# Optimization experiments

Measured on AMD Instinct MI355X. Metric: run time of the kernel, lower is better.

Reference implementation:

```python
import jax, jax.numpy as jnp
import numpy as np

B, D, H, L = 16384, 512, 1024, 2


def _lstm_step_zero_state(x, W_ih, W_hh, b_ih, b_hh):
    """One PyTorch-convention LSTM cell step with h0=c0=0.

    Gate order: i, f, g, o. With h0=0 the W_hh matmul contributes nothing,
    but both biases still apply (matches cuDNN/PyTorch math exactly).
    With c0=0 the forget-gate term f*c0 vanishes.
    x: (B, in), W_ih: (4H, in), W_hh: (4H, H), biases: (4H,)
    """
    gates = x @ W_ih.T + (b_ih + b_hh)  # (B, 4H)
    i, f, g, o = jnp.split(gates, 4, axis=-1)
    i = jax.nn.sigmoid(i)
    g = jnp.tanh(g)
    o = jax.nn.sigmoid(o)
    c = i * g  # f * c0 == 0
    h = o * jnp.tanh(c)
    return h


def setup_inputs() -> dict:
    key = jax.random.key(0)
    ks = jax.random.split(key, 12)
    s = 1.0 / np.sqrt(H)  # PyTorch LSTM init scale

    def u(k, shape):
        return jax.random.uniform(k, shape, jnp.float32, -s, s)

    x = jax.random.normal(ks[0], (B, D), jnp.float32)
    return {
        "x": x,
        "W_ih0": u(ks[1], (4 * H, D)),
        "W_hh0": u(ks[2], (4 * H, H)),
        "b_ih0": u(ks[3], (4 * H,)),
        "b_hh0": u(ks[4], (4 * H,)),
        "W_ih1": u(ks[5], (4 * H, H)),
        "W_hh1": u(ks[6], (4 * H, H)),
        "b_ih1": u(ks[7], (4 * H,)),
        "b_hh1": u(ks[8], (4 * H,)),
        "W_dec": u(ks[9], (D, H)),
        "b_dec": u(ks[10], (D,)),
    }


def reference(x, W_ih0, W_hh0, b_ih0, b_hh0, W_ih1, W_hh1, b_ih1, b_hh1, W_dec, b_dec):
    # forward(): x.unsqueeze(1) -> 2-layer LSTM (zero init state, 1 step) -> decoder
    h0 = _lstm_step_zero_state(x, W_ih0, W_hh0, b_ih0, b_hh0)   # (B, H)
    h1 = _lstm_step_zero_state(h0, W_ih1, W_hh1, b_ih1, b_hh1)  # (B, H)
    return h1 @ W_dec.T + b_dec  # (B, D)
```

## Files before the change

### kernel.cpp

```cpp
#include <hip/hip_runtime.h>
#include <stdint.h>


typedef __attribute__((ext_vector_type(8))) __bf16 bf16x8;
typedef __attribute__((ext_vector_type(8))) unsigned short u16x8;
typedef __attribute__((ext_vector_type(4))) float f32x4;

#define BM 128
#define BK 64

__device__ __forceinline__ unsigned short f2b(float f) {
    unsigned int x = __builtin_bit_cast(unsigned int, f);
    x = x + 0x7FFFu + ((x >> 16) & 1u);
    return (unsigned short)(x >> 16);
}
__device__ __forceinline__ float sigf(float x) { return 1.0f / (1.0f + __expf(-x)); }
__device__ __forceinline__ float tanh_safe(float x) {
    float a = fabsf(x);
    float e = __expf(-2.0f * a);
    float t = (1.0f - e) / (1.0f + e);
    return x < 0.0f ? -t : t;
}

__device__ __forceinline__ void cvt8(const float* __restrict__ s,
                                     unsigned short* __restrict__ d) {
    f32x4 lo = *reinterpret_cast<const f32x4*>(s);
    f32x4 hi = *reinterpret_cast<const f32x4*>(s + 4);
    u16x8 v;
    v[0] = f2b(lo[0]); v[1] = f2b(lo[1]); v[2] = f2b(lo[2]); v[3] = f2b(lo[3]);
    v[4] = f2b(hi[0]); v[5] = f2b(hi[1]); v[6] = f2b(hi[2]); v[7] = f2b(hi[3]);
    *reinterpret_cast<u16x8*>(d) = v;
}

__device__ __forceinline__ void gload16(const void* g, void* l) {
    __builtin_amdgcn_global_load_lds(
        (const __attribute__((address_space(1))) void*)g,
        (__attribute__((address_space(3))) void*)l,
        16, 0, 0);
}

__global__ __launch_bounds__(256) void cvt_lin(const float* __restrict__ s,
                                               unsigned short* __restrict__ d,
                                               int n8) {
    int stride = gridDim.x * blockDim.x;
    for (int c = blockIdx.x * blockDim.x + threadIdx.x; c < n8; c += stride)
        cvt8(s + (size_t)c * 8, d + (size_t)c * 8);
}

__global__ __launch_bounds__(256) void pack_w(const float* __restrict__ W,
                                              unsigned short* __restrict__ d,
                                              int K8, int H, int n8) {
    int stride = gridDim.x * blockDim.x;
    for (int c = blockIdx.x * blockDim.x + threadIdx.x; c < n8; c += stride) {
        int dstRow = c / K8, kc = c - dstRow * K8;
        int group = dstRow / 96, r = dstRow - group * 96;
        int gate = (r % 48) >> 4;
        int goff = (gate == 0) ? 0 : (gate + 1);
        int hcol = group * 32 + (r / 48) * 16 + (r & 15);
        cvt8(W + ((size_t)(goff * H + hcol) * K8 + kc) * 8, d + (size_t)c * 8);
    }
}

template <int GATED, int AK, int BMODE, int NF>
__global__ __launch_bounds__(256) void gemm_fused(
    const void* __restrict__ Av,
    const void* __restrict__ Wv,
    const float* __restrict__ b0,
    const float* __restrict__ b1,
    void* __restrict__ Ov,
    int M, int K, int N, int NBX)
{
    constexpr int WCS   = NF * 16;
    constexpr int BROWS = NF * 32;
    constexpr int ONB   = GATED ? 32 : BROWS;

    __shared__ __align__(16) unsigned short sA[BM * BK];
    __shared__ __align__(16) unsigned short sB[BROWS * BK];

    const int tid  = threadIdx.x;
    const int lane = tid & 63;
    const int w    = tid >> 6;
    const int wr   = w >> 1, wc = w & 1;
    const int l16  = lane & 15, hi8 = lane >> 4;

    const int cpx  = gridDim.x >> 3;
    const int orig = blockIdx.x;
    const int rid  = (orig & 7) * cpx + (orig >> 3);
    const int bx   = rid % NBX;
    const int by   = rid / NBX;

    const int row0 = by * BM;
    const int n0   = bx * ONB;

    const unsigned short* gA16[4];
    const float*          gA32[4];
    unsigned short*       lA[4];
#pragma unroll
    for (int i = 0; i < 4; ++i) {
        int ch = tid + i * 256, r = ch >> 3, slot = ch & 7, ls = slot ^ (r & 7);
        if constexpr (AK) {
            lA[i]   = sA + ch * 8;
            gA16[i] = (const unsigned short*)Av + (size_t)(row0 + r) * K + ls * 8;
        } else {
            lA[i]   = sA + r * BK + ls * 8;
            gA32[i] = (const float*)Av + (size_t)(row0 + r) * K + slot * 8;
        }
    }
    const unsigned short* gB16[NF];
    const float*          gB32[NF];
    unsigned short*       lB[NF];
#pragma unroll
    for (int i = 0; i < NF; ++i) {
        int ch = tid + i * 256, r = ch >> 3, slot = ch & 7, ls = slot ^ (r & 7);
        if constexpr (BMODE) {
            lB[i]   = sB + ch * 8;
            int prow = GATED ? bx * BROWS + r : n0 + r;
            gB16[i] = (const unsigned short*)Wv + (size_t)prow * K + ls * 8;
        } else {
            lB[i] = sB + r * BK + ls * 8;
            int wrow;
            if (GATED) {
                int gate = (r % WCS) >> 4;
                int goff = (gate == 0) ? 0 : (gate + 1);
                int hcol = n0 + (r / WCS) * 16 + (r & 15);
                wrow = goff * N + hcol;
            } else {
                wrow = n0 + r;
            }
            gB32[i] = (const float*)Wv + (size_t)wrow * K + slot * 8;
        }
    }

    f32x4 acc[4][NF];
#pragma unroll
    for (int m = 0; m < 4; ++m)
#pragma unroll
        for (int n = 0; n < NF; ++n)
            acc[m][n] = (f32x4){0.f, 0.f, 0.f, 0.f};

    for (int k0 = 0; k0 < K; k0 += BK) {
#pragma unroll
        for (int i = 0; i < 4; ++i) {
            if constexpr (AK) gload16(gA16[i] + k0, lA[i]);
            else              cvt8(gA32[i] + k0, lA[i]);
        }
#pragma unroll
        for (int i = 0; i < NF; ++i) {
            if constexpr (BMODE) gload16(gB16[i] + k0, lB[i]);
            else                 cvt8(gB32[i] + k0, lB[i]);
        }
        __syncthreads();

#pragma unroll
        for (int ks = 0; ks < 2; ++ks) {
            bf16x8 av[4], bv[NF];
#pragma unroll
            for (int m = 0; m < 4; ++m) {
                int row = wr * 64 + m * 16 + l16;
                int ps = (ks * 4 + hi8) ^ (row & 7);
                av[m] = *reinterpret_cast<const bf16x8*>(sA + row * BK + ps * 8);
            }
#pragma unroll
            for (int n = 0; n < NF; ++n) {
                int row = wc * WCS + n * 16 + l16;
                int ps = (ks * 4 + hi8) ^ (row & 7);
                bv[n] = *reinterpret_cast<const bf16x8*>(sB + row * BK + ps * 8);
            }
#pragma unroll
            for (int m = 0; m < 4; ++m)
#pragma unroll
                for (int n = 0; n < NF; ++n)
                    acc[m][n] = __builtin_amdgcn_mfma_f32_16x16x32_bf16(
                        av[m], bv[n], acc[m][n], 0, 0, 0);
        }
        __syncthreads();
    }

    if constexpr (GATED) {
        unsigned short* O = (unsigned short*)Ov;
        const int hcol = n0 + wc * 16 + l16;
        const float bi = b0[hcol]         + b1[hcol];
        const float bg = b0[2 * N + hcol] + b1[2 * N + hcol];
        const float bo = b0[3 * N + hcol] + b1[3 * N + hcol];
#pragma unroll
        for (int m = 0; m < 4; ++m) {
            int rbase = row0 + wr * 64 + m * 16 + hi8 * 4;
#pragma unroll
            for (int q = 0; q < 4; ++q) {
                float iv = sigf(acc[m][0][q] + bi);
                float gv = tanh_safe(acc[m][1][q] + bg);
                float ov = sigf(acc[m][2][q] + bo);
                float h  = ov * tanh_safe(iv * gv);
                O[(size_t)(rbase + q) * N + hcol] = f2b(h);
            }
        }
    } else {
        float* O = (float*)Ov;
#pragma unroll
        for (int n = 0; n < NF; ++n) {
            int col = n0 + wc * WCS + n * 16 + l16;
            float bias = b0[col];
#pragma unroll
            for (int m = 0; m < 4; ++m) {
                int rbase = row0 + wr * 64 + m * 16 + hi8 * 4;
#pragma unroll
                for (int q = 0; q < 4; ++q)
                    O[(size_t)(rbase + q) * N + col] = acc[m][n][q] + bias;
            }
        }
    }
}

extern "C" void kernel_launch(void* const* d_in, const int* in_sizes, int n_in,
                              void* d_out, int out_size, void* d_ws, size_t ws_size,
                              hipStream_t stream) {
    constexpr int M = 16384, D = 512, H = 1024;

    const float* x    = (const float*)d_in[0];
    const float* Wih0 = (const float*)d_in[1];
    const float* bih0 = (const float*)d_in[3];
    const float* bhh0 = (const float*)d_in[4];
    const float* Wih1 = (const float*)d_in[5];
    const float* bih1 = (const float*)d_in[7];
    const float* bhh1 = (const float*)d_in[8];
    const float* Wdec = (const float*)d_in[9];
    const float* bdec = (const float*)d_in[10];

    const size_t szH = (size_t)M * H * 2;
    const size_t sw0 = (size_t)3 * H * D * 2;
    const size_t sw1 = (size_t)3 * H * H * 2;
    const size_t swd = (size_t)D * H * 2;

    unsigned short* h0 = (unsigned short*)d_ws;
    unsigned short* h1 = (unsigned short*)((char*)d_ws + szH);
    unsigned short* xb = h1;
    unsigned short* wp0   = (unsigned short*)((char*)d_ws + 2 * szH);
    unsigned short* wp1   = (unsigned short*)((char*)wp0 + sw0);
    unsigned short* wdecb = (unsigned short*)((char*)wp1 + sw1);

    const bool packed = ws_size >= 2 * szH + sw0 + sw1 + swd;

    if (packed) {
        cvt_lin<<<2048, 256, 0, stream>>>(x, xb, M * D / 8);
        pack_w <<<768,  256, 0, stream>>>(Wih0, wp0, D / 8, H, 3 * H * D / 8);
        pack_w <<<1536, 256, 0, stream>>>(Wih1, wp1, H / 8, H, 3 * H * H / 8);
        cvt_lin<<<256,  256, 0, stream>>>(Wdec, wdecb, D * H / 8);

        gemm_fused<1, 1, 1, 3><<<dim3((H / 32) * (M / BM)), 256, 0, stream>>>(
            xb, wp0, bih0, bhh0, h0, M, D, H, H / 32);
        gemm_fused<1, 1, 1, 3><<<dim3((H / 32) * (M / BM)), 256, 0, stream>>>(
            h0, wp1, bih1, bhh1, h1, M, H, H, H / 32);
        gemm_fused<0, 1, 1, 2><<<dim3((D / 64) * (M / BM)), 256, 0, stream>>>(
            h1, wdecb, bdec, nullptr, (float*)d_out, M, H, D, D / 64);
    } else {
        gemm_fused<1, 0, 0, 3><<<dim3((H / 32) * (M / BM)), 256, 0, stream>>>(
            x, Wih0, bih0, bhh0, h0, M, D, H, H / 32);
        gemm_fused<1, 1, 0, 3><<<dim3((H / 32) * (M / BM)), 256, 0, stream>>>(
            h0, Wih1, bih1, bhh1, h1, M, H, H, H / 32);
        gemm_fused<0, 1, 0, 2><<<dim3((D / 64) * (M / BM)), 256, 0, stream>>>(
            h1, Wdec, bdec, nullptr, (float*)d_out, M, H, D, D / 64);
    }
}
```

Baseline: 252.3 us.

## Double-buffer LDS with async loads and enlarge GEMM tiles to 256-row, 512-thread blocks

Switches the fused GEMM to 512-thread blocks with a 256-row M tile and wider N tiles per block. Shared-memory A and B buffers are double-buffered, and the next tiles are prefetched with explicit vmcnt waits so global-to-LDS loads overlap MFMA work. MFMA priority is raised with s_setprio. The weight packing layout is adjusted to the new 64-column gate groups, and the unpacked fallback path is removed, so a large enough workspace is now assumed. Larger tiles raise register and LDS pressure, and the grid shrinks, which may lower occupancy and load balance.

```diff
diff --git a/kernel.cpp b/kernel.cpp
--- a/kernel.cpp
+++ b/kernel.cpp
@@ -6,7 +6,7 @@
 typedef __attribute__((ext_vector_type(8))) unsigned short u16x8;
 typedef __attribute__((ext_vector_type(4))) float f32x4;
 
-#define BM 128
+#define BM 256
 #define BK 64
 
 __device__ __forceinline__ unsigned short f2b(float f) {
@@ -53,34 +53,35 @@
     int stride = gridDim.x * blockDim.x;
     for (int c = blockIdx.x * blockDim.x + threadIdx.x; c < n8; c += stride) {
         int dstRow = c / K8, kc = c - dstRow * K8;
-        int group = dstRow / 96, r = dstRow - group * 96;
-        int gate = (r % 48) >> 4;
+        int group = dstRow / 192, r = dstRow - group * 192;
+        int wc = r / 48, rr = r - wc * 48;
+        int gate = rr >> 4;
         int goff = (gate == 0) ? 0 : (gate + 1);
-        int hcol = group * 32 + (r / 48) * 16 + (r & 15);
+        int hcol = group * 64 + wc * 16 + (rr & 15);
         cvt8(W + ((size_t)(goff * H + hcol) * K8 + kc) * 8, d + (size_t)c * 8);
     }
 }
 
-template <int GATED, int AK, int BMODE, int NF>
-__global__ __launch_bounds__(256) void gemm_fused(
-    const void* __restrict__ Av,
-    const void* __restrict__ Wv,
+template <int GATED, int NF>
+__global__ __launch_bounds__(512, 1) void gemm_fused(
+    const unsigned short* __restrict__ A,
+    const unsigned short* __restrict__ Wp,
     const float* __restrict__ b0,
     const float* __restrict__ b1,
     void* __restrict__ Ov,
     int M, int K, int N, int NBX)
 {
-    constexpr int WCS   = NF * 16;
-    constexpr int BROWS = NF * 32;
-    constexpr int ONB   = GATED ? 32 : BROWS;
-
-    __shared__ __align__(16) unsigned short sA[BM * BK];
-    __shared__ __align__(16) unsigned short sB[BROWS * BK];
+    constexpr int BROWS = NF * 64;
+    constexpr int WNS   = NF * 16;
+    constexpr int ONB   = GATED ? 64 : 128;
+
+    __shared__ __align__(16) unsigned short sA[2][BM * BK];
+    __shared__ __align__(16) unsigned short sB[2][BROWS * BK];
 
     const int tid  = threadIdx.x;
     const int lane = tid & 63;
     const int w    = tid >> 6;
-    const int wr   = w >> 1, wc = w & 1;
+    const int wr   = w >> 2, wc = w & 3;
     const int l16  = lane & 15, hi8 = lane >> 4;
 
     const int cpx  = gridDim.x >> 3;
@@ -88,92 +89,85 @@
     const int rid  = (orig & 7) * cpx + (orig >> 3);
     const int bx   = rid % NBX;
     const int by   = rid / NBX;
-
     const int row0 = by * BM;
     const int n0   = bx * ONB;
 
-    const unsigned short* gA16[4];
-    const float*          gA32[4];
-    unsigned short*       lA[4];
+    const unsigned short* pA[4]; int dA[4];
 #pragma unroll
     for (int i = 0; i < 4; ++i) {
-        int ch = tid + i * 256, r = ch >> 3, slot = ch & 7, ls = slot ^ (r & 7);
-        if constexpr (AK) {
-            lA[i]   = sA + ch * 8;
-            gA16[i] = (const unsigned short*)Av + (size_t)(row0 + r) * K + ls * 8;
-        } else {
-            lA[i]   = sA + r * BK + ls * 8;
-            gA32[i] = (const float*)Av + (size_t)(row0 + r) * K + slot * 8;
-        }
-    }
-    const unsigned short* gB16[NF];
-    const float*          gB32[NF];
-    unsigned short*       lB[NF];
+        int ch = tid + i * 512, r = ch >> 3, slot = ch & 7, ls = slot ^ (r & 7);
+        dA[i] = ch * 8;
+        pA[i] = A + (size_t)(row0 + r) * K + ls * 8;
+    }
+    const unsigned short* pB[NF]; int dB[NF];
 #pragma unroll
     for (int i = 0; i < NF; ++i) {
-        int ch = tid + i * 256, r = ch >> 3, slot = ch & 7, ls = slot ^ (r & 7);
-        if constexpr (BMODE) {
-            lB[i]   = sB + ch * 8;
-            int prow = GATED ? bx * BROWS + r : n0 + r;
-            gB16[i] = (const unsigned short*)Wv + (size_t)prow * K + ls * 8;
-        } else {
-            lB[i] = sB + r * BK + ls * 8;
-            int wrow;
-            if (GATED) {
-                int gate = (r % WCS) >> 4;
-                int goff = (gate == 0) ? 0 : (gate + 1);
-                int hcol = n0 + (r / WCS) * 16 + (r & 15);
-                wrow = goff * N + hcol;
-            } else {
-                wrow = n0 + r;
-            }
-            gB32[i] = (const float*)Wv + (size_t)wrow * K + slot * 8;
-        }
-    }
-
-    f32x4 acc[4][NF];
-#pragma unroll
-    for (int m = 0; m < 4; ++m)
+        int ch = tid + i * 512, r = ch >> 3, slot = ch & 7, ls = slot ^ (r & 7);
+        dB[i] = ch * 8;
+        int prow = GATED ? bx * BROWS + r : n0 + r;
+        pB[i] = Wp + (size_t)prow * K + ls * 8;
+    }
+
+    auto issue = [&](int buf) {
+#pragma unroll
+        for (int i = 0; i < 4; ++i)  { gload16(pA[i], &sA[buf][dA[i]]); pA[i] += BK; }
+#pragma unroll
+        for (int i = 0; i < NF; ++i) { gload16(pB[i], &sB[buf][dB[i]]); pB[i] += BK; }
+    };
+
+    f32x4 acc[8][NF];
+#pragma unroll
+    for (int m = 0; m < 8; ++m)
 #pragma unroll
         for (int n = 0; n < NF; ++n)
             acc[m][n] = (f32x4){0.f, 0.f, 0.f, 0.f};
 
-    for (int k0 = 0; k0 < K; k0 += BK) {
-#pragma unroll
-        for (int i = 0; i < 4; ++i) {
-            if constexpr (AK) gload16(gA16[i] + k0, lA[i]);
-            else              cvt8(gA32[i] + k0, lA[i]);
-        }
-#pragma unroll
-        for (int i = 0; i < NF; ++i) {
-            if constexpr (BMODE) gload16(gB16[i] + k0, lB[i]);
-            else                 cvt8(gB32[i] + k0, lB[i]);
-        }
-        __syncthreads();
-
+    const int NT = K >> 6;
+    issue(0);
+    issue(1);
+    int cur = 0;
+
+    for (int t = 0; t < NT; ++t) {
+        if (t + 1 < NT) {
+            if constexpr (NF == 3) asm volatile("s_waitcnt vmcnt(7)" ::: "memory");
+            else                   asm volatile("s_waitcnt vmcnt(6)" ::: "memory");
+        } else {
+            asm volatile("s_waitcnt vmcnt(0)" ::: "memory");
+        }
+        __builtin_amdgcn_sched_barrier(0);
+        __builtin_amdgcn_s_barrier();
+
+        const unsigned short* sAc = sA[cur];
+        const unsigned short* sBc = sB[cur];
 #pragma unroll
         for (int ks = 0; ks < 2; ++ks) {
-            bf16x8 av[4], bv[NF];
-#pragma unroll
-            for (int m = 0; m < 4; ++m) {
-                int row = wr * 64 + m * 16 + l16;
+            bf16x8 av[8], bv[NF];
+#pragma unroll
+            for (int m = 0; m < 8; ++m) {
+                int row = wr * 128 + m * 16 + l16;
                 int ps = (ks * 4 + hi8) ^ (row & 7);
-                av[m] = *reinterpret_cast<const bf16x8*>(sA + row * BK + ps * 8);
+                av[m] = *reinterpret_cast<const bf16x8*>(sAc + row * BK + ps * 8);
             }
 #pragma unroll
             for (int n = 0; n < NF; ++n) {
-                int row = wc * WCS + n * 16 + l16;
+                int row = wc * WNS + n * 16 + l16;
                 int ps = (ks * 4 + hi8) ^ (row & 7);
-                bv[n] = *reinterpret_cast<const bf16x8*>(sB + row * BK + ps * 8);
-            }
-#pragma unroll
-            for (int m = 0; m < 4; ++m)
+                bv[n] = *reinterpret_cast<const bf16x8*>(sBc + row * BK + ps * 8);
+            }
+            __builtin_amdgcn_s_setprio(1);
+#pragma unroll
+            for (int m = 0; m < 8; ++m)
 #pragma unroll
                 for (int n = 0; n < NF; ++n)
                     acc[m][n] = __builtin_amdgcn_mfma_f32_16x16x32_bf16(
                         av[m], bv[n], acc[m][n], 0, 0, 0);
-        }
-        __syncthreads();
+            __builtin_amdgcn_s_setprio(0);
+        }
+        asm volatile("s_waitcnt lgkmcnt(0)" ::: "memory");
+        __builtin_amdgcn_sched_barrier(0);
+        __builtin_amdgcn_s_barrier();
+        if (t + 2 < NT) issue(cur);
+        cur ^= 1;
     }
 
     if constexpr (GATED) {
@@ -183,8 +177,8 @@
         const float bg = b0[2 * N + hcol] + b1[2 * N + hcol];
         const float bo = b0[3 * N + hcol] + b1[3 * N + hcol];
 #pragma unroll
-        for (int m = 0; m < 4; ++m) {
-            int rbase = row0 + wr * 64 + m * 16 + hi8 * 4;
+        for (int m = 0; m < 8; ++m) {
+            int rbase = row0 + wr * 128 + m * 16 + hi8 * 4;
 #pragma unroll
             for (int q = 0; q < 4; ++q) {
                 float iv = sigf(acc[m][0][q] + bi);
@@ -198,11 +192,11 @@
         float* O = (float*)Ov;
 #pragma unroll
         for (int n = 0; n < NF; ++n) {
-            int col = n0 + wc * WCS + n * 16 + l16;
+            int col = n0 + wc * WNS + n * 16 + l16;
             float bias = b0[col];
 #pragma unroll
-            for (int m = 0; m < 4; ++m) {
-                int rbase = row0 + wr * 64 + m * 16 + hi8 * 4;
+            for (int m = 0; m < 8; ++m) {
+                int rbase = row0 + wr * 128 + m * 16 + hi8 * 4;
 #pragma unroll
                 for (int q = 0; q < 4; ++q)
                     O[(size_t)(rbase + q) * N + col] = acc[m][n][q] + bias;
@@ -229,7 +223,6 @@
     const size_t szH = (size_t)M * H * 2;
     const size_t sw0 = (size_t)3 * H * D * 2;
     const size_t sw1 = (size_t)3 * H * H * 2;
-    const size_t swd = (size_t)D * H * 2;
 
     unsigned short* h0 = (unsigned short*)d_ws;
     unsigned short* h1 = (unsigned short*)((char*)d_ws + szH);
@@ -238,26 +231,15 @@
     unsigned short* wp1   = (unsigned short*)((char*)wp0 + sw0);
     unsigned short* wdecb = (unsigned short*)((char*)wp1 + sw1);
 
-    const bool packed = ws_size >= 2 * szH + sw0 + sw1 + swd;
-
-    if (packed) {
-        cvt_lin<<<2048, 256, 0, stream>>>(x, xb, M * D / 8);
-        pack_w <<<768,  256, 0, stream>>>(Wih0, wp0, D / 8, H, 3 * H * D / 8);
-        pack_w <<<1536, 256, 0, stream>>>(Wih1, wp1, H / 8, H, 3 * H * H / 8);
-        cvt_lin<<<256,  256, 0, stream>>>(Wdec, wdecb, D * H / 8);
-
-        gemm_fused<1, 1, 1, 3><<<dim3((H / 32) * (M / BM)), 256, 0, stream>>>(
-            xb, wp0, bih0, bhh0, h0, M, D, H, H / 32);
-        gemm_fused<1, 1, 1, 3><<<dim3((H / 32) * (M / BM)), 256, 0, stream>>>(
-            h0, wp1, bih1, bhh1, h1, M, H, H, H / 32);
-        gemm_fused<0, 1, 1, 2><<<dim3((D / 64) * (M / BM)), 256, 0, stream>>>(
-            h1, wdecb, bdec, nullptr, (float*)d_out, M, H, D, D / 64);
-    } else {
-        gemm_fused<1, 0, 0, 3><<<dim3((H / 32) * (M / BM)), 256, 0, stream>>>(
-            x, Wih0, bih0, bhh0, h0, M, D, H, H / 32);
-        gemm_fused<1, 1, 0, 3><<<dim3((H / 32) * (M / BM)), 256, 0, stream>>>(
-            h0, Wih1, bih1, bhh1, h1, M, H, H, H / 32);
-        gemm_fused<0, 1, 0, 2><<<dim3((D / 64) * (M / BM)), 256, 0, stream>>>(
-            h1, Wdec, bdec, nullptr, (float*)d_out, M, H, D, D / 64);
-    }
-}
+    cvt_lin<<<2048, 256, 0, stream>>>(x, xb, M * D / 8);
+    pack_w <<<768,  256, 0, stream>>>(Wih0, wp0, D / 8, H, 3 * H * D / 8);
+    pack_w <<<1536, 256, 0, stream>>>(Wih1, wp1, H / 8, H, 3 * H * H / 8);
+    cvt_lin<<<256,  256, 0, stream>>>(Wdec, wdecb, D * H / 8);
+
+    gemm_fused<1, 3><<<dim3((H / 64) * (M / BM)), 512, 0, stream>>>(
+        xb, wp0, bih0, bhh0, h0, M, D, H, H / 64);
+    gemm_fused<1, 3><<<dim3((H / 64) * (M / BM)), 512, 0, stream>>>(
+        h0, wp1, bih1, bhh1, h1, M, H, H, H / 64);
+    gemm_fused<0, 2><<<dim3((D / 128) * (M / BM)), 512, 0, stream>>>(
+        h1, wdecb, bdec, nullptr, (float*)d_out, M, H, D, D / 128);
+}
```

After: 274.6 us. 8.8% more time.

## Widen GEMM output tiles to 64 hidden / 128 cols and simplify loads

Applied to the files above, without the earlier changes.

Each block now covers 64 hidden units (192 packed weight rows) in the gated GEMMs and 128 output columns in the decoder GEMM, up from 32 and 64. The weight packing is changed to match the wider tile layout. This improves A-tile reuse per block and halves the number of blocks, aiming to cut global/LDS traffic for the activation matrix. The fp32 fallback path is removed, loads are driven by 32-bit offsets, and launch_bounds now requests 3 waves per SIMD. The trade-off is higher register pressure from more accumulators and fewer blocks in flight.

```diff
diff --git a/kernel.cpp b/kernel.cpp
--- a/kernel.cpp
+++ b/kernel.cpp
@@ -3,7 +3,6 @@
 
 
 typedef __attribute__((ext_vector_type(8))) __bf16 bf16x8;
-typedef __attribute__((ext_vector_type(8))) unsigned short u16x8;
 typedef __attribute__((ext_vector_type(4))) float f32x4;
 
 #define BM 128
@@ -26,13 +25,13 @@
                                      unsigned short* __restrict__ d) {
     f32x4 lo = *reinterpret_cast<const f32x4*>(s);
     f32x4 hi = *reinterpret_cast<const f32x4*>(s + 4);
-    u16x8 v;
+    __attribute__((ext_vector_type(8))) unsigned short v;
     v[0] = f2b(lo[0]); v[1] = f2b(lo[1]); v[2] = f2b(lo[2]); v[3] = f2b(lo[3]);
     v[4] = f2b(hi[0]); v[5] = f2b(hi[1]); v[6] = f2b(hi[2]); v[7] = f2b(hi[3]);
-    *reinterpret_cast<u16x8*>(d) = v;
-}
-
-__device__ __forceinline__ void gload16(const void* g, void* l) {
+    *reinterpret_cast<__attribute__((ext_vector_type(8))) unsigned short*>(d) = v;
+}
+
+__device__ __forceinline__ void gload16(const unsigned short* g, unsigned short* l) {
     __builtin_amdgcn_global_load_lds(
         (const __attribute__((address_space(1))) void*)g,
         (__attribute__((address_space(3))) void*)l,
@@ -53,26 +52,30 @@
     int stride = gridDim.x * blockDim.x;
     for (int c = blockIdx.x * blockDim.x + threadIdx.x; c < n8; c += stride) {
         int dstRow = c / K8, kc = c - dstRow * K8;
-        int group = dstRow / 96, r = dstRow - group * 96;
-        int gate = (r % 48) >> 4;
+        int G = dstRow / 192, r = dstRow - G * 192;
+        int wc = r / 96, rr = r - wc * 96;
+        int n = rr >> 4, i = rr & 15;
+        int hsub = n / 3, gate = n - hsub * 3;
         int goff = (gate == 0) ? 0 : (gate + 1);
-        int hcol = group * 32 + (r / 48) * 16 + (r & 15);
+        int hcol = G * 64 + wc * 32 + hsub * 16 + i;
         cvt8(W + ((size_t)(goff * H + hcol) * K8 + kc) * 8, d + (size_t)c * 8);
     }
 }
 
-template <int GATED, int AK, int BMODE, int NF>
-__global__ __launch_bounds__(256) void gemm_fused(
-    const void* __restrict__ Av,
-    const void* __restrict__ Wv,
+template <int GATED>
+__global__ __launch_bounds__(256, 3) void gemm_fused(
+    const unsigned short* __restrict__ A,
+    const unsigned short* __restrict__ Wp,
     const float* __restrict__ b0,
     const float* __restrict__ b1,
     void* __restrict__ Ov,
     int M, int K, int N, int NBX)
 {
-    constexpr int WCS   = NF * 16;
-    constexpr int BROWS = NF * 32;
-    constexpr int ONB   = GATED ? 32 : BROWS;
+    constexpr int NFR   = GATED ? 6 : 4;
+    constexpr int BROWS = GATED ? 192 : 128;
+    constexpr int WCS   = GATED ? 96 : 64;
+    constexpr int ONB   = GATED ? 64 : 128;
+    constexpr int NBCH  = BROWS / 32;
 
     __shared__ __align__(16) unsigned short sA[BM * BK];
     __shared__ __align__(16) unsigned short sB[BROWS * BK];
@@ -88,72 +91,35 @@
     const int rid  = (orig & 7) * cpx + (orig >> 3);
     const int bx   = rid % NBX;
     const int by   = rid / NBX;
-
     const int row0 = by * BM;
     const int n0   = bx * ONB;
 
-    const unsigned short* gA16[4];
-    const float*          gA32[4];
-    unsigned short*       lA[4];
-#pragma unroll
-    for (int i = 0; i < 4; ++i) {
-        int ch = tid + i * 256, r = ch >> 3, slot = ch & 7, ls = slot ^ (r & 7);
-        if constexpr (AK) {
-            lA[i]   = sA + ch * 8;
-            gA16[i] = (const unsigned short*)Av + (size_t)(row0 + r) * K + ls * 8;
-        } else {
-            lA[i]   = sA + r * BK + ls * 8;
-            gA32[i] = (const float*)Av + (size_t)(row0 + r) * K + slot * 8;
-        }
-    }
-    const unsigned short* gB16[NF];
-    const float*          gB32[NF];
-    unsigned short*       lB[NF];
-#pragma unroll
-    for (int i = 0; i < NF; ++i) {
-        int ch = tid + i * 256, r = ch >> 3, slot = ch & 7, ls = slot ^ (r & 7);
-        if constexpr (BMODE) {
-            lB[i]   = sB + ch * 8;
-            int prow = GATED ? bx * BROWS + r : n0 + r;
-            gB16[i] = (const unsigned short*)Wv + (size_t)prow * K + ls * 8;
-        } else {
-            lB[i] = sB + r * BK + ls * 8;
-            int wrow;
-            if (GATED) {
-                int gate = (r % WCS) >> 4;
-                int goff = (gate == 0) ? 0 : (gate + 1);
-                int hcol = n0 + (r / WCS) * 16 + (r & 15);
-                wrow = goff * N + hcol;
-            } else {
-                wrow = n0 + r;
-            }
-            gB32[i] = (const float*)Wv + (size_t)wrow * K + slot * 8;
-        }
-    }
-
-    f32x4 acc[4][NF];
+    const int r0 = tid >> 3, sl = tid & 7;
+    const int ls = sl ^ (r0 & 7);
+    const unsigned int strd = 32u * (unsigned)K;
+    unsigned int offA = (unsigned)(row0 + r0) * (unsigned)K + ls * 8;
+    unsigned int offB = (unsigned)(GATED ? bx * BROWS + r0 : n0 + r0)
+                        * (unsigned)K + ls * 8;
+
+    f32x4 acc[4][NFR];
 #pragma unroll
     for (int m = 0; m < 4; ++m)
 #pragma unroll
-        for (int n = 0; n < NF; ++n)
+        for (int n = 0; n < NFR; ++n)
             acc[m][n] = (f32x4){0.f, 0.f, 0.f, 0.f};
 
     for (int k0 = 0; k0 < K; k0 += BK) {
 #pragma unroll
-        for (int i = 0; i < 4; ++i) {
-            if constexpr (AK) gload16(gA16[i] + k0, lA[i]);
-            else              cvt8(gA32[i] + k0, lA[i]);
-        }
-#pragma unroll
-        for (int i = 0; i < NF; ++i) {
-            if constexpr (BMODE) gload16(gB16[i] + k0, lB[i]);
-            else                 cvt8(gB32[i] + k0, lB[i]);
-        }
+        for (int i = 0; i < 4; ++i)
+            gload16(A + offA + i * strd + k0, sA + tid * 8 + i * 2048);
+#pragma unroll
+        for (int i = 0; i < NBCH; ++i)
+            gload16(Wp + offB + i * strd + k0, sB + tid * 8 + i * 2048);
         __syncthreads();
 
 #pragma unroll
         for (int ks = 0; ks < 2; ++ks) {
-            bf16x8 av[4], bv[NF];
+            bf16x8 av[4], bv[NFR];
 #pragma unroll
             for (int m = 0; m < 4; ++m) {
                 int row = wr * 64 + m * 16 + l16;
@@ -161,7 +127,7 @@
                 av[m] = *reinterpret_cast<const bf16x8*>(sA + row * BK + ps * 8);
             }
 #pragma unroll
-            for (int n = 0; n < NF; ++n) {
+            for (int n = 0; n < NFR; ++n) {
                 int row = wc * WCS + n * 16 + l16;
                 int ps = (ks * 4 + hi8) ^ (row & 7);
                 bv[n] = *reinterpret_cast<const bf16x8*>(sB + row * BK + ps * 8);
@@ -169,7 +135,7 @@
 #pragma unroll
             for (int m = 0; m < 4; ++m)
 #pragma unroll
-                for (int n = 0; n < NF; ++n)
+                for (int n = 0; n < NFR; ++n)
                     acc[m][n] = __builtin_amdgcn_mfma_f32_16x16x32_bf16(
                         av[m], bv[n], acc[m][n], 0, 0, 0);
         }
@@ -178,26 +144,29 @@
 
     if constexpr (GATED) {
         unsigned short* O = (unsigned short*)Ov;
-        const int hcol = n0 + wc * 16 + l16;
-        const float bi = b0[hcol]         + b1[hcol];
-        const float bg = b0[2 * N + hcol] + b1[2 * N + hcol];
-        const float bo = b0[3 * N + hcol] + b1[3 * N + hcol];
-#pragma unroll
-        for (int m = 0; m < 4; ++m) {
-            int rbase = row0 + wr * 64 + m * 16 + hi8 * 4;
-#pragma unroll
-            for (int q = 0; q < 4; ++q) {
-                float iv = sigf(acc[m][0][q] + bi);
-                float gv = tanh_safe(acc[m][1][q] + bg);
-                float ov = sigf(acc[m][2][q] + bo);
-                float h  = ov * tanh_safe(iv * gv);
-                O[(size_t)(rbase + q) * N + hcol] = f2b(h);
+#pragma unroll
+        for (int hsub = 0; hsub < 2; ++hsub) {
+            const int hcol = n0 + wc * 32 + hsub * 16 + l16;
+            const float bi = b0[hcol]         + b1[hcol];
+            const float bg = b0[2 * N + hcol] + b1[2 * N + hcol];
+            const float bo = b0[3 * N + hcol] + b1[3 * N + hcol];
+#pragma unroll
+            for (int m = 0; m < 4; ++m) {
+                int rbase = row0 + wr * 64 + m * 16 + hi8 * 4;
+#pragma unroll
+                for (int q = 0; q < 4; ++q) {
+                    float iv = sigf(acc[m][hsub * 3 + 0][q] + bi);
+                    float gv = tanh_safe(acc[m][hsub * 3 + 1][q] + bg);
+                    float ov = sigf(acc[m][hsub * 3 + 2][q] + bo);
+                    float h  = ov * tanh_safe(iv * gv);
+                    O[(size_t)(rbase + q) * N + hcol] = f2b(h);
+                }
             }
         }
     } else {
         float* O = (float*)Ov;
 #pragma unroll
-        for (int n = 0; n < NF; ++n) {
+        for (int n = 0; n < NFR; ++n) {
             int col = n0 + wc * WCS + n * 16 + l16;
             float bias = b0[col];
 #pragma unroll
@@ -229,7 +198,6 @@
     const size_t szH = (size_t)M * H * 2;
     const size_t sw0 = (size_t)3 * H * D * 2;
     const size_t sw1 = (size_t)3 * H * H * 2;
-    const size_t swd = (size_t)D * H * 2;
 
     unsigned short* h0 = (unsigned short*)d_ws;
     unsigned short* h1 = (unsigned short*)((char*)d_ws + szH);
@@ -238,26 +206,15 @@
     unsigned short* wp1   = (unsigned short*)((char*)wp0 + sw0);
     unsigned short* wdecb = (unsigned short*)((char*)wp1 + sw1);
 
-    const bool packed = ws_size >= 2 * szH + sw0 + sw1 + swd;
-
-    if (packed) {
-        cvt_lin<<<2048, 256, 0, stream>>>(x, xb, M * D / 8);
-        pack_w <<<768,  256, 0, stream>>>(Wih0, wp0, D / 8, H, 3 * H * D / 8);
-        pack_w <<<1536, 256, 0, stream>>>(Wih1, wp1, H / 8, H, 3 * H * H / 8);
-        cvt_lin<<<256,  256, 0, stream>>>(Wdec, wdecb, D * H / 8);
-
-        gemm_fused<1, 1, 1, 3><<<dim3((H / 32) * (M / BM)), 256, 0, stream>>>(
-            xb, wp0, bih0, bhh0, h0, M, D, H, H / 32);
-        gemm_fused<1, 1, 1, 3><<<dim3((H / 32) * (M / BM)), 256, 0, stream>>>(
-            h0, wp1, bih1, bhh1, h1, M, H, H, H / 32);
-        gemm_fused<0, 1, 1, 2><<<dim3((D / 64) * (M / BM)), 256, 0, stream>>>(
-            h1, wdecb, bdec, nullptr, (float*)d_out, M, H, D, D / 64);
-    } else {
-        gemm_fused<1, 0, 0, 3><<<dim3((H / 32) * (M / BM)), 256, 0, stream>>>(
-            x, Wih0, bih0, bhh0, h0, M, D, H, H / 32);
-        gemm_fused<1, 1, 0, 3><<<dim3((H / 32) * (M / BM)), 256, 0, stream>>>(
-            h0, Wih1, bih1, bhh1, h1, M, H, H, H / 32);
-        gemm_fused<0, 1, 0, 2><<<dim3((D / 64) * (M / BM)), 256, 0, stream>>>(
-            h1, Wdec, bdec, nullptr, (float*)d_out, M, H, D, D / 64);
-    }
-}
+    cvt_lin<<<2048, 256, 0, stream>>>(x, xb, M * D / 8);
+    pack_w <<<768,  256, 0, stream>>>(Wih0, wp0, D / 8, H, 3 * H * D / 8);
+    pack_w <<<1536, 256, 0, stream>>>(Wih1, wp1, H / 8, H, 3 * H * H / 8);
+    cvt_lin<<<256,  256, 0, stream>>>(Wdec, wdecb, D * H / 8);
+
+    gemm_fused<1><<<dim3((H / 64) * (M / BM)), 256, 0, stream>>>(
+        xb, wp0, bih0, bhh0, h0, M, D, H, H / 64);
+    gemm_fused<1><<<dim3((H / 64) * (M / BM)), 256, 0, stream>>>(
+        h0, wp1, bih1, bhh1, h1, M, H, H, H / 64);
+    gemm_fused<0><<<dim3((D / 128) * (M / BM)), 256, 0, stream>>>(
+        h1, wdecb, bdec, nullptr, (float*)d_out, M, H, D, D / 128);
+}
```

After: 215.6 us. -14.6%, faster.
